# Optimization experiments

Measured on AMD Instinct MI355X. Metric: run time of the kernel, lower is better.

The kernel has to match this reference:

```python
import jax, jax.numpy as jnp
import numpy as np

EMBED_DIM = 768
NUM_HEADS = 12
HEAD_DIM = EMBED_DIM // NUM_HEADS
BSZ = 2
SEQ = 2048


def setup_inputs() -> dict:
    key = jax.random.key(0)
    ks = jax.random.split(key, 8)
    w = lambda k: (jax.random.normal(k, (EMBED_DIM, EMBED_DIM), jnp.float32) * 0.02)
    return {
        "hidden_states": jax.random.normal(ks[0], (BSZ, SEQ, EMBED_DIM), jnp.float32),
        "attention_mask": jnp.zeros((BSZ, 1, SEQ, SEQ), jnp.float32),
        "attention_bias": jax.random.normal(ks[1], (BSZ * NUM_HEADS, SEQ), jnp.float32),
        "Wq": w(ks[2]), "bq": jnp.zeros((EMBED_DIM,), jnp.float32),
        "Wk": w(ks[3]), "bk": jnp.zeros((EMBED_DIM,), jnp.float32),
        "Wv": w(ks[4]), "bv": jnp.zeros((EMBED_DIM,), jnp.float32),
        "Wo": w(ks[5]), "bo": jnp.zeros((EMBED_DIM,), jnp.float32),
        "beta": jnp.ones((1,), jnp.float32),
        "beta_bias": jnp.zeros((1,), jnp.float32),
    }


def reference(hidden_states, attention_mask, attention_bias, Wq, bq, Wk, bk, Wv, bv, Wo, bo, beta, beta_bias):
    b, t, e = hidden_states.shape
    scaling = HEAD_DIM ** -0.5
    split = lambda x: x.reshape(b, t, NUM_HEADS, HEAD_DIM).transpose(0, 2, 1, 3)  # b h t d
    q = split(hidden_states @ Wq.T + bq) * scaling
    k = split(hidden_states @ Wk.T + bk)
    v = split(hidden_states @ Wv.T + bv)
    # scores: [b, h, t, s]
    scores = jnp.einsum('bhqd,bhkd->bhqk', q, k)
    bias = attention_bias.reshape(b, NUM_HEADS, 1, t)  # (bsz*nh, src) -> broadcast over queries
    scores = scores + beta * bias + beta_bias + attention_mask
    probs = jax.nn.softmax(scores, axis=-1)
    out = jnp.einsum('bhqk,bhkd->bhqd', probs, v)  # b h t d
    out = out.transpose(0, 2, 1, 3).reshape(b, t, e)
    return out @ Wo.T + bo
```

## Files before the change

kernel.cpp:

```cpp
#include <hip/hip_runtime.h>
#include <hip/hip_bf16.h>

#define E 768
#define HD 64
#define NH 12
#define BSZ 2
#define SEQ 2048
#define M_ROWS (BSZ * SEQ)
#define BH (BSZ * NH)

#define LOG2E 1.44269504f
#define QSCALE 0.18033688f
#define MSHIFT 16.0f

typedef float f4_t __attribute__((ext_vector_type(4)));
typedef float f32x16 __attribute__((ext_vector_type(16)));
typedef __bf16 bf8_t __attribute__((ext_vector_type(8)));
typedef unsigned short us8_t __attribute__((ext_vector_type(8)));
typedef unsigned short us4_t __attribute__((ext_vector_type(4)));

__device__ inline unsigned short f2bf(float f) {
  union { float f; unsigned u; } v; v.f = f;
  unsigned u = v.u + 0x7FFFu + ((v.u >> 16) & 1u);
  return (unsigned short)(u >> 16);
}

__device__ inline float ex2(float x) { return __builtin_amdgcn_exp2f(x); }

__device__ inline float bflo(unsigned u) { union { unsigned u; float f; } v; v.u = u << 16; return v.f; }
__device__ inline float bfhi(unsigned u) { union { unsigned u; float f; } v; v.u = u & 0xFFFF0000u; return v.f; }

__device__ inline unsigned pk2(float a, float b) {
  union { float f; unsigned u; } ua, ub;
  ua.f = a; ub.f = b;
  return __builtin_amdgcn_perm(ub.u + 0x8000u, ua.u + 0x8000u, 0x07060302u);
}

__device__ inline void swap32(unsigned& a, unsigned& b) {
  asm volatile("v_permlane32_swap_b32 %0, %1" : "+v"(a), "+v"(b));
}

__global__ __launch_bounds__(256) void cvt_all(
    const float* __restrict__ X, const float* __restrict__ Wq,
    const float* __restrict__ Wk, const float* __restrict__ Wv,
    const float* __restrict__ Wo, const float* __restrict__ mask,
    const float* __restrict__ abias, const float* __restrict__ betaP,
    const float* __restrict__ bbiasP,
    unsigned short* __restrict__ Xbf, unsigned short* __restrict__ Wqkv,
    unsigned short* __restrict__ Wobf, unsigned short* __restrict__ maskbf,
    float* __restrict__ biasPf) {
  const int nW = E * E;
  int id = blockIdx.x;
  if (id < 2688) {
    const float* src;
    unsigned short* dst;
    float scale = 1.0f;
    int base;
    if (id < 1536) {
      src = X; dst = Xbf; base = id * 2048;
    } else {
      int r = id - 1536;
      int k = r / 288;
      int rb = r - k * 288;
      base = rb * 2048;
      if (k == 0)      { src = Wq; dst = Wqkv;          scale = QSCALE; }
      else if (k == 1) { src = Wk; dst = Wqkv + nW;     }
      else if (k == 2) { src = Wv; dst = Wqkv + 2 * nW; }
      else             { src = Wo; dst = Wobf;          }
    }
    int i = base + threadIdx.x * 8;
    const float4* s = (const float4*)(src + i);
    float4 a = s[0], b = s[1];
    us8_t o;
    o[0] = f2bf(a.x * scale); o[1] = f2bf(a.y * scale);
    o[2] = f2bf(a.z * scale); o[3] = f2bf(a.w * scale);
    o[4] = f2bf(b.x * scale); o[5] = f2bf(b.y * scale);
    o[6] = f2bf(b.z * scale); o[7] = f2bf(b.w * scale);
    *(us8_t*)(dst + i) = o;
    return;
  }
  if (id < 6784) {
    int rowid = id - 2688;
    int bb = rowid >> 11, q = rowid & 2047;
    int s0 = threadIdx.x * 8;
    const float4* s = (const float4*)(mask + (size_t)rowid * 2048 + s0);
    float4 a = s[0], c = s[1];
    int tile = s0 >> 6, kk = s0 & 63;
    int base = ((bb * 32 + tile) * 2048 + q) * 64 + (kk >> 5) * 32 + ((kk & 31) >> 3) * 4;
    us4_t lo, hi4;
    lo[0] = f2bf(a.x * LOG2E); lo[1] = f2bf(a.y * LOG2E);
    lo[2] = f2bf(a.z * LOG2E); lo[3] = f2bf(a.w * LOG2E);
    hi4[0] = f2bf(c.x * LOG2E); hi4[1] = f2bf(c.y * LOG2E);
    hi4[2] = f2bf(c.z * LOG2E); hi4[3] = f2bf(c.w * LOG2E);
    *(us4_t*)(maskbf + base) = lo;
    *(us4_t*)(maskbf + base + 16) = hi4;
    return;
  }
  {
    int bh = id - 6784;
    int s0 = threadIdx.x * 8;
    const float4* s = (const float4*)(abias + (size_t)bh * 2048 + s0);
    float4 a = s[0], c = s[1];
    float bv = LOG2E * betaP[0];
    float bc = LOG2E * bbiasP[0] - MSHIFT;
    int tile = s0 >> 6, kk = s0 & 63;
    int base = bh * 2048 + tile * 64 + (kk >> 5) * 32 + ((kk & 31) >> 3) * 4;
    f4_t lo = {fmaf(bv, a.x, bc), fmaf(bv, a.y, bc), fmaf(bv, a.z, bc), fmaf(bv, a.w, bc)};
    f4_t hi4 = {fmaf(bv, c.x, bc), fmaf(bv, c.y, bc), fmaf(bv, c.z, bc), fmaf(bv, c.w, bc)};
    *(f4_t*)(biasPf + base) = lo;
    *(f4_t*)(biasPf + base + 16) = hi4;
  }
}

__global__ __launch_bounds__(256) void gemm_qkv(
    const unsigned short* __restrict__ A, const unsigned short* __restrict__ Bw,
    const float* __restrict__ bq, const float* __restrict__ bk, const float* __restrict__ bv,
    unsigned short* __restrict__ Qb, unsigned short* __restrict__ Kb,
    unsigned short* __restrict__ Vtb) {
  __shared__ unsigned short Alds[64 * 64];
  __shared__ unsigned short Blds[128 * 64];
  const int w = threadIdx.x >> 6, lane = threadIdx.x & 63;
  const int quad = lane >> 4, l15 = lane & 15;
  const int rowBase = blockIdx.x * 64;
  const int colBase = blockIdx.y * 128;
  const int wr = (w & 1) * 32, wc = (w >> 1) * 64;
  f4_t acc[2][4] = {};
  const int swz = l15 & 7;

  for (int k0 = 0; k0 < E; k0 += 64) {
    __syncthreads();
#pragma unroll
    for (int c = 0; c < 2; ++c) {
      int s = c * 256 + w * 64 + lane;
      int r = s >> 3, col = ((s & 7) ^ (r & 7)) * 8;
      const unsigned short* ga = A + (size_t)(rowBase + r) * E + k0 + col;
      __builtin_amdgcn_global_load_lds((const __attribute__((address_space(1))) void*)ga,
          (__attribute__((address_space(3))) void*)&Alds[c * 2048 + w * 512], 16, 0, 0);
    }
#pragma unroll
    for (int c = 0; c < 4; ++c) {
      int s = c * 256 + w * 64 + lane;
      int r = s >> 3, col = ((s & 7) ^ (r & 7)) * 8;
      const unsigned short* gb = Bw + (size_t)(colBase + r) * E + k0 + col;
      __builtin_amdgcn_global_load_lds((const __attribute__((address_space(1))) void*)gb,
          (__attribute__((address_space(3))) void*)&Blds[c * 2048 + w * 512], 16, 0, 0);
    }
    __builtin_amdgcn_s_waitcnt(0);
    __syncthreads();
    bf8_t af[2][2], bfr[4][2];
#pragma unroll
    for (int mi = 0; mi < 2; ++mi)
#pragma unroll
      for (int ks = 0; ks < 2; ++ks)
        af[mi][ks] = *(const bf8_t*)&Alds[(wr + mi * 16 + l15) * 64 + (((ks * 4 + quad) ^ swz) << 3)];
#pragma unroll
    for (int ni = 0; ni < 4; ++ni)
#pragma unroll
      for (int ks = 0; ks < 2; ++ks)
        bfr[ni][ks] = *(const bf8_t*)&Blds[(wc + ni * 16 + l15) * 64 + (((ks * 4 + quad) ^ swz) << 3)];
#pragma unroll
    for (int ks = 0; ks < 2; ++ks)
#pragma unroll
      for (int mi = 0; mi < 2; ++mi)
#pragma unroll
        for (int ni = 0; ni < 4; ++ni)
          acc[mi][ni] = __builtin_amdgcn_mfma_f32_16x16x32_bf16(af[mi][ks], bfr[ni][ks], acc[mi][ni], 0, 0, 0);
  }

  const int which = colBase / E;
  __syncthreads();
  if (which < 2) {
    const float* biasP = (which == 0) ? bq : bk;
    unsigned short* dst = (which == 0) ? Qb : Kb;
    const float bscale = (which == 0) ? QSCALE : 1.0f;
    const int cnBase = colBase - which * E + wc;
    const int h = cnBase >> 6;
    float biasv[4];
#pragma unroll
    for (int ni = 0; ni < 4; ++ni) biasv[ni] = biasP[cnBase + ni * 16 + l15] * bscale;
    unsigned short* T = Blds + w * 1024;
    const int row = lane >> 2, colE = (lane & 3) * 16;
#pragma unroll
    for (int mi = 0; mi < 2; ++mi) {
#pragma unroll
      for (int ni = 0; ni < 4; ++ni)
#pragma unroll
        for (int r = 0; r < 4; ++r)
          T[(quad * 4 + r) * 64 + ni * 16 + l15] = f2bf(acc[mi][ni][r] + biasv[ni]);
      us8_t o0 = *(const us8_t*)&T[row * 64 + colE];
      us8_t o1 = *(const us8_t*)&T[row * 64 + colE + 8];
      int gm = rowBase + wr + mi * 16 + row;
      int b = gm >> 11, t = gm & 2047;
      unsigned short* drow = dst + ((size_t)(b * NH + h) * SEQ + t) * HD;
      *(us8_t*)&drow[colE] = o0;
      *(us8_t*)&drow[colE + 8] = o1;
    }
  } else {
#pragma unroll
    for (int mi = 0; mi < 2; ++mi) {
#pragma unroll
      for (int ni = 0; ni < 4; ++ni) {
        int cn = colBase - 2 * E + wc + ni * 16 + l15;
        int h = cn >> 6, d = cn & 63;
        float bias = bv[cn];
        int gm0 = rowBase + wr + mi * 16 + quad * 4;
        int b = gm0 >> 11, t = gm0 & 2047;
        us4_t o4;
#pragma unroll
        for (int r = 0; r < 4; ++r) o4[r] = f2bf(acc[mi][ni][r] + bias);
        *(us4_t*)&Vtb[((size_t)(b * NH + h) * HD + d) * SEQ + t] = o4;
      }
    }
  }
}

__device__ inline void addBM(f32x16& SA, const float* bp, us8_t ma, us8_t mb) {
  union { us8_t s; unsigned u[4]; } ca, cb;
  ca.s = ma; cb.s = mb;
#pragma unroll
  for (int g = 0; g < 4; ++g) {
    f4_t bw = *(const f4_t*)(bp + g * 4);
    unsigned wl = (g < 2) ? ca.u[2 * g] : cb.u[2 * g - 4];
    unsigned wh = (g < 2) ? ca.u[2 * g + 1] : cb.u[2 * g - 3];
    SA[4 * g + 0] += bw[0] + bflo(wl);
    SA[4 * g + 1] += bw[1] + bfhi(wl);
    SA[4 * g + 2] += bw[2] + bflo(wh);
    SA[4 * g + 3] += bw[3] + bfhi(wh);
  }
}

__device__ inline void packP(f32x16& SA, float& L, bf8_t& F0, bf8_t& F1) {
#pragma unroll
  for (int r = 0; r < 16; ++r) {
    SA[r] = ex2(SA[r]);
    L += SA[r];
  }
  unsigned u0 = pk2(SA[0], SA[1]), u1 = pk2(SA[2], SA[3]);
  unsigned u2 = pk2(SA[4], SA[5]), u3 = pk2(SA[6], SA[7]);
  unsigned u4 = pk2(SA[8], SA[9]), u5 = pk2(SA[10], SA[11]);
  unsigned u6 = pk2(SA[12], SA[13]), u7 = pk2(SA[14], SA[15]);
  swap32(u0, u2); swap32(u1, u3); swap32(u4, u6); swap32(u5, u7);
  union { unsigned u[4]; bf8_t b; } fa, fb;
  fa.u[0] = u0; fa.u[1] = u1; fa.u[2] = u2; fa.u[3] = u3;
  fb.u[0] = u4; fb.u[1] = u5; fb.u[2] = u6; fb.u[3] = u7;
  F0 = fa.b; F1 = fb.b;
}

__global__ __launch_bounds__(256, 3) void flash_attn12(
    const unsigned short* __restrict__ Qb, const unsigned short* __restrict__ Kb,
    const unsigned short* __restrict__ Vt, const unsigned short* __restrict__ maskP,
    const float* __restrict__ biasPf, unsigned short* __restrict__ attn) {
  __shared__ __align__(16) char smem[40960];
  const int tid = threadIdx.x;
  const int w = tid >> 6, lane = tid & 63;
  const int l31 = lane & 31, hi = lane >> 5;
  const int p = w >> 1, qw = (w & 1) * 32;
  const int id = blockIdx.x;
  const int h = id >> 6;
  const int qb = id & 63;
  const int qt = qb >> 1, b = qb & 1;
  const int bh = b * NH + h;
  const int q0 = qt * 64;
  const int q = q0 + qw + l31;

  unsigned short* KldsP = (unsigned short*)(smem + p * 16384);
  unsigned short* VldsP = KldsP + 4096;
  float* biasF = (float*)(smem + 32768);

  {
    const float* srcB = biasPf + bh * 2048 + tid * 8;
    f4_t b0 = *(const f4_t*)srcB;
    f4_t b1 = *(const f4_t*)(srcB + 4);
    *(f4_t*)&biasF[tid * 8] = b0;
    *(f4_t*)&biasF[tid * 8 + 4] = b1;
  }

  bf8_t qf[4];
  {
    const unsigned short* qbase = Qb + ((size_t)bh * SEQ + q) * HD + hi * 8;
#pragma unroll
    for (int dk = 0; dk < 4; ++dk) qf[dk] = *(const bf8_t*)(qbase + dk * 16);
  }

  const int li = (w & 1) * 64 + lane;
  const int r0 = li >> 3, cc = li & 7;
  const int dstOff = r0 * 64 + ((cc ^ (r0 & 7)) << 3);
  const unsigned short* KgBase = Kb + (size_t)bh * SEQ * HD;
  const unsigned short* VtG = Vt + (size_t)bh * HD * SEQ;
  const unsigned short* kSrc = KgBase + (p * 1024 + r0) * 64 + cc * 8;
  const unsigned short* vSrc = VtG + r0 * SEQ + p * 1024 + cc * 8;
  const unsigned short* mSrc = maskP + (((size_t)(b * 32 + p * 16) * 2048) + q) * 64 + hi * 16;

  us8_t kpf0, kpf1, kpf2, kpf3, vpf0, vpf1, vpf2, vpf3, mpf0, mpf1, mpf2, mpf3;

#define PF_KV(T)                                                              \
  {                                                                           \
    const unsigned short* kp_ = kSrc + (T) * 4096;                            \
    const unsigned short* vp_ = vSrc + (T) * 64;                              \
    asm volatile("global_load_dwordx4 %0, %4, off\n\t"                        \
                 "global_load_dwordx4 %1, %5, off\n\t"                        \
                 "global_load_dwordx4 %2, %6, off\n\t"                        \
                 "global_load_dwordx4 %3, %7, off"                            \
                 : "=&v"(kpf0), "=&v"(kpf1), "=&v"(kpf2), "=&v"(kpf3)         \
                 : "v"(kp_), "v"(kp_ + 1024), "v"(kp_ + 2048), "v"(kp_ + 3072)); \
    asm volatile("global_load_dwordx4 %0, %4, off\n\t"                        \
                 "global_load_dwordx4 %1, %5, off\n\t"                        \
                 "global_load_dwordx4 %2, %6, off\n\t"                        \
                 "global_load_dwordx4 %3, %7, off"                            \
                 : "=&v"(vpf0), "=&v"(vpf1), "=&v"(vpf2), "=&v"(vpf3)         \
                 : "v"(vp_), "v"(vp_ + 16 * SEQ), "v"(vp_ + 32 * SEQ),        \
                   "v"(vp_ + 48 * SEQ));                                      \
  }

#define PF_M(T)                                                               \
  {                                                                           \
    const unsigned short* mp_ = mSrc + (size_t)(T) * 131072;                  \
    asm volatile("global_load_dwordx4 %0, %4, off\n\t"                        \
                 "global_load_dwordx4 %1, %5, off\n\t"                        \
                 "global_load_dwordx4 %2, %6, off\n\t"                        \
                 "global_load_dwordx4 %3, %7, off"                            \
                 : "=&v"(mpf0), "=&v"(mpf1), "=&v"(mpf2), "=&v"(mpf3)         \
                 : "v"(mp_), "v"(mp_ + 8), "v"(mp_ + 32), "v"(mp_ + 40));     \
  }

  PF_KV(0);
  PF_M(0);

  f32x16 Oacc0 = {}, Oacc1 = {};
  float Lacc = 0.0f;
  const int swzA = l31 & 7;

  for (int it = 0; it < 16; ++it) {
    asm volatile("s_waitcnt vmcnt(4)"
                 : "+v"(kpf0), "+v"(kpf1), "+v"(kpf2), "+v"(kpf3),
                   "+v"(vpf0), "+v"(vpf1), "+v"(vpf2), "+v"(vpf3));
    __syncthreads();
    {
      us8_t* kd = (us8_t*)(KldsP + dstOff);
      kd[0] = kpf0; kd[128] = kpf1; kd[256] = kpf2; kd[384] = kpf3;
      us8_t* vd = (us8_t*)(VldsP + dstOff);
      vd[0] = vpf0; vd[128] = vpf1; vd[256] = vpf2; vd[384] = vpf3;
    }
    __syncthreads();

    f32x16 s0 = {}, s1 = {};
    __builtin_amdgcn_s_setprio(1);
#pragma unroll
    for (int dk = 0; dk < 4; ++dk) {
      const int co = ((dk * 2 + hi) ^ swzA) << 3;
      bf8_t k0 = *(const bf8_t*)(KldsP + l31 * 64 + co);
      bf8_t k1 = *(const bf8_t*)(KldsP + (32 + l31) * 64 + co);
      s0 = __builtin_amdgcn_mfma_f32_32x32x16_bf16(k0, qf[dk], s0, 0, 0, 0);
      s1 = __builtin_amdgcn_mfma_f32_32x32x16_bf16(k1, qf[dk], s1, 0, 0, 0);
    }
    __builtin_amdgcn_s_setprio(0);

    if (it < 15) {
      PF_KV(it + 1);
      asm volatile("s_waitcnt vmcnt(8)"
                   : "+v"(mpf0), "+v"(mpf1), "+v"(mpf2), "+v"(mpf3));
    } else {
      asm volatile("s_waitcnt vmcnt(0)"
                   : "+v"(mpf0), "+v"(mpf1), "+v"(mpf2), "+v"(mpf3));
    }

    const float* bp = biasF + ((p << 4) + it) * 64 + (hi << 4);
    addBM(s0, bp, mpf0, mpf1);
    addBM(s1, bp + 32, mpf2, mpf3);

    if (it < 15) PF_M(it + 1);

    bf8_t pfr0, pfr1, pfr2, pfr3;
    packP(s0, Lacc, pfr0, pfr1);
    packP(s1, Lacc, pfr2, pfr3);

    __builtin_amdgcn_s_setprio(1);
#pragma unroll
    for (int ks = 0; ks < 4; ++ks) {
      const int co = ((ks * 2 + hi) ^ swzA) << 3;
      bf8_t v0 = *(const bf8_t*)(VldsP + l31 * 64 + co);
      bf8_t v1 = *(const bf8_t*)(VldsP + (32 + l31) * 64 + co);
      bf8_t pp = ks == 0 ? pfr0 : ks == 1 ? pfr1 : ks == 2 ? pfr2 : pfr3;
      Oacc0 = __builtin_amdgcn_mfma_f32_32x32x16_bf16(v0, pp, Oacc0, 0, 0, 0);
      Oacc1 = __builtin_amdgcn_mfma_f32_32x32x16_bf16(v1, pp, Oacc1, 0, 0, 0);
    }
    __builtin_amdgcn_s_setprio(0);
  }

  __syncthreads();
  {
    float* OfP = (float*)smem + p * (64 * 65);
    const int qr = (qw + l31) * 65;
#pragma unroll
    for (int r = 0; r < 16; ++r) {
      int d = (r & 3) + 8 * (r >> 2) + 4 * hi;
      OfP[qr + d] = Oacc0[r];
      OfP[qr + 32 + d] = Oacc1[r];
    }
    float Lf = Lacc + __shfl_xor(Lacc, 32);
    if (hi == 0) OfP[qr + 64] = Lf;
  }
  __syncthreads();
  {
    const float* O0 = (const float*)smem;
    const float* O1 = O0 + 64 * 65;
    const int ql = tid >> 2, dc = tid & 3;
    const int qr = ql * 65;
    float inv = 1.0f / (O0[qr + 64] + O1[qr + 64]);
    unsigned short* orow = attn + ((size_t)b * SEQ + q0 + ql) * E + h * HD + dc * 16;
    us8_t o0, o1;
#pragma unroll
    for (int i = 0; i < 8; ++i)
      o0[i] = f2bf((O0[qr + dc * 16 + i] + O1[qr + dc * 16 + i]) * inv);
#pragma unroll
    for (int i = 0; i < 8; ++i)
      o1[i] = f2bf((O0[qr + dc * 16 + 8 + i] + O1[qr + dc * 16 + 8 + i]) * inv);
    *(us8_t*)orow = o0;
    *(us8_t*)(orow + 8) = o1;
  }
}

__global__ __launch_bounds__(256) void gemm_out(
    const unsigned short* __restrict__ A, const unsigned short* __restrict__ Bw,
    const float* __restrict__ bo, float* __restrict__ out) {
  __shared__ unsigned short Alds[64 * 64];
  __shared__ unsigned short Blds[64 * 64];
  const int w = threadIdx.x >> 6, lane = threadIdx.x & 63;
  const int quad = lane >> 4, l15 = lane & 15;
  const int rowBase = blockIdx.x * 64;
  const int colBase = blockIdx.y * 64;
  const int wr = (w & 1) * 32, wc = (w >> 1) * 32;
  f4_t acc[2][2] = {};
  const int swz = l15 & 7;

  for (int k0 = 0; k0 < E; k0 += 64) {
    __syncthreads();
#pragma unroll
    for (int c = 0; c < 2; ++c) {
      int s = c * 256 + w * 64 + lane;
      int r = s >> 3, col = ((s & 7) ^ (r & 7)) * 8;
      const unsigned short* ga = A + (size_t)(rowBase + r) * E + k0 + col;
      __builtin_amdgcn_global_load_lds((const __attribute__((address_space(1))) void*)ga,
          (__attribute__((address_space(3))) void*)&Alds[c * 2048 + w * 512], 16, 0, 0);
      const unsigned short* gb = Bw + (size_t)(colBase + r) * E + k0 + col;
      __builtin_amdgcn_global_load_lds((const __attribute__((address_space(1))) void*)gb,
          (__attribute__((address_space(3))) void*)&Blds[c * 2048 + w * 512], 16, 0, 0);
    }
    __builtin_amdgcn_s_waitcnt(0);
    __syncthreads();
    bf8_t af[2][2], bfr[2][2];
#pragma unroll
    for (int mi = 0; mi < 2; ++mi)
#pragma unroll
      for (int ks = 0; ks < 2; ++ks)
        af[mi][ks] = *(const bf8_t*)&Alds[(wr + mi * 16 + l15) * 64 + (((ks * 4 + quad) ^ swz) << 3)];
#pragma unroll
    for (int ni = 0; ni < 2; ++ni)
#pragma unroll
      for (int ks = 0; ks < 2; ++ks)
        bfr[ni][ks] = *(const bf8_t*)&Blds[(wc + ni * 16 + l15) * 64 + (((ks * 4 + quad) ^ swz) << 3)];
#pragma unroll
    for (int ks = 0; ks < 2; ++ks)
#pragma unroll
      for (int mi = 0; mi < 2; ++mi)
#pragma unroll
        for (int ni = 0; ni < 2; ++ni)
          acc[mi][ni] = __builtin_amdgcn_mfma_f32_16x16x32_bf16(af[mi][ks], bfr[ni][ks], acc[mi][ni], 0, 0, 0);
  }

#pragma unroll
  for (int mi = 0; mi < 2; ++mi) {
#pragma unroll
    for (int ni = 0; ni < 2; ++ni) {
      int gn = colBase + wc + ni * 16 + l15;
      float bias = bo[gn];
#pragma unroll
      for (int r = 0; r < 4; ++r) {
        int gm = rowBase + wr + mi * 16 + quad * 4 + r;
        out[(size_t)gm * E + gn] = acc[mi][ni][r] + bias;
      }
    }
  }
}

extern "C" void kernel_launch(void* const* d_in, const int* in_sizes, int n_in,
                              void* d_out, int out_size, void* d_ws, size_t ws_size,
                              hipStream_t stream) {
  const float* hidden = (const float*)d_in[0];
  const float* mask = (const float*)d_in[1];
  const float* abias = (const float*)d_in[2];
  const float* Wq = (const float*)d_in[3];
  const float* bq = (const float*)d_in[4];
  const float* Wk = (const float*)d_in[5];
  const float* bk = (const float*)d_in[6];
  const float* Wv = (const float*)d_in[7];
  const float* bv = (const float*)d_in[8];
  const float* Wo = (const float*)d_in[9];
  const float* bo = (const float*)d_in[10];
  const float* beta = (const float*)d_in[11];
  const float* betaBias = (const float*)d_in[12];
  float* out = (float*)d_out;

  char* ws = (char*)d_ws;
  unsigned short* Xbf = (unsigned short*)(ws);
  unsigned short* Wqkv = (unsigned short*)(ws + 6291456);
  unsigned short* Wobf = (unsigned short*)(ws + 9830400);
  unsigned short* Qbuf = (unsigned short*)(ws + 11010048);
  unsigned short* Kbuf = (unsigned short*)(ws + 17301504);
  unsigned short* Vtb = (unsigned short*)(ws + 23592960);
  unsigned short* Maskbf = (unsigned short*)(ws + 29884416);
  float* BiasP = (float*)(ws + 46661632);
  unsigned short* Attn = Xbf;

  cvt_all<<<6808, 256, 0, stream>>>(hidden, Wq, Wk, Wv, Wo, mask, abias, beta, betaBias,
                                    Xbf, Wqkv, Wobf, Maskbf, BiasP);
  gemm_qkv<<<dim3(64, 18), 256, 0, stream>>>(Xbf, Wqkv, bq, bk, bv, Qbuf, Kbuf, Vtb);
  flash_attn12<<<768, 256, 0, stream>>>(Qbuf, Kbuf, Vtb, Maskbf, BiasP, Attn);
  gemm_out<<<dim3(64, 12), 256, 0, stream>>>(Attn, Wobf, bo, out);
}
```

Before: 194.6 us.

## Read fp32 mask directly in attention; double-buffer LDS in both GEMMs

Removes the separate mask conversion pass, which wrote a bf16 tiled copy of the full mask, so the attention kernel now streams the fp32 mask straight from global memory and folds LOG2E scaling into the score initialisation, issuing mask loads before the QK MFMAs. This drops one full write and re-read of a large intermediate, at the cost of reading fp32 (twice the bytes) inside attention. The QKV and output GEMMs gain LDS double buffering so the next K-tile's global-to-LDS loads overlap the current MFMAs. The K/V prefetch is also reorganised with offset addressing and its wait points are moved.

New measurement: 245.4 us. +26.2%, slower.

```diff
diff --git a/kernel.cpp b/kernel.cpp
--- a/kernel.cpp
+++ b/kernel.cpp
@@ -27,9 +27,6 @@
 
 __device__ inline float ex2(float x) { return __builtin_amdgcn_exp2f(x); }
 
-__device__ inline float bflo(unsigned u) { union { unsigned u; float f; } v; v.u = u << 16; return v.f; }
-__device__ inline float bfhi(unsigned u) { union { unsigned u; float f; } v; v.u = u & 0xFFFF0000u; return v.f; }
-
 __device__ inline unsigned pk2(float a, float b) {
   union { float f; unsigned u; } ua, ub;
   ua.f = a; ub.f = b;
@@ -43,12 +40,10 @@
 __global__ __launch_bounds__(256) void cvt_all(
     const float* __restrict__ X, const float* __restrict__ Wq,
     const float* __restrict__ Wk, const float* __restrict__ Wv,
-    const float* __restrict__ Wo, const float* __restrict__ mask,
-    const float* __restrict__ abias, const float* __restrict__ betaP,
-    const float* __restrict__ bbiasP,
+    const float* __restrict__ Wo, const float* __restrict__ abias,
+    const float* __restrict__ betaP, const float* __restrict__ bbiasP,
     unsigned short* __restrict__ Xbf, unsigned short* __restrict__ Wqkv,
-    unsigned short* __restrict__ Wobf, unsigned short* __restrict__ maskbf,
-    float* __restrict__ biasPf) {
+    unsigned short* __restrict__ Wobf, float* __restrict__ biasPf) {
   const int nW = E * E;
   int id = blockIdx.x;
   if (id < 2688) {
@@ -79,25 +74,8 @@
     *(us8_t*)(dst + i) = o;
     return;
   }
-  if (id < 6784) {
-    int rowid = id - 2688;
-    int bb = rowid >> 11, q = rowid & 2047;
-    int s0 = threadIdx.x * 8;
-    const float4* s = (const float4*)(mask + (size_t)rowid * 2048 + s0);
-    float4 a = s[0], c = s[1];
-    int tile = s0 >> 6, kk = s0 & 63;
-    int base = ((bb * 32 + tile) * 2048 + q) * 64 + (kk >> 5) * 32 + ((kk & 31) >> 3) * 4;
-    us4_t lo, hi4;
-    lo[0] = f2bf(a.x * LOG2E); lo[1] = f2bf(a.y * LOG2E);
-    lo[2] = f2bf(a.z * LOG2E); lo[3] = f2bf(a.w * LOG2E);
-    hi4[0] = f2bf(c.x * LOG2E); hi4[1] = f2bf(c.y * LOG2E);
-    hi4[2] = f2bf(c.z * LOG2E); hi4[3] = f2bf(c.w * LOG2E);
-    *(us4_t*)(maskbf + base) = lo;
-    *(us4_t*)(maskbf + base + 16) = hi4;
-    return;
-  }
   {
-    int bh = id - 6784;
+    int bh = id - 2688;
     int s0 = threadIdx.x * 8;
     const float4* s = (const float4*)(abias + (size_t)bh * 2048 + s0);
     float4 a = s[0], c = s[1];
@@ -117,8 +95,8 @@
     const float* __restrict__ bq, const float* __restrict__ bk, const float* __restrict__ bv,
     unsigned short* __restrict__ Qb, unsigned short* __restrict__ Kb,
     unsigned short* __restrict__ Vtb) {
-  __shared__ unsigned short Alds[64 * 64];
-  __shared__ unsigned short Blds[128 * 64];
+  __shared__ unsigned short Alds[2][64 * 64];
+  __shared__ unsigned short Blds[2][128 * 64];
   const int w = threadIdx.x >> 6, lane = threadIdx.x & 63;
   const int quad = lane >> 4, l15 = lane & 15;
   const int rowBase = blockIdx.x * 64;
@@ -127,48 +105,57 @@
   f4_t acc[2][4] = {};
   const int swz = l15 & 7;
 
-  for (int k0 = 0; k0 < E; k0 += 64) {
-    __syncthreads();
-#pragma unroll
-    for (int c = 0; c < 2; ++c) {
-      int s = c * 256 + w * 64 + lane;
-      int r = s >> 3, col = ((s & 7) ^ (r & 7)) * 8;
-      const unsigned short* ga = A + (size_t)(rowBase + r) * E + k0 + col;
-      __builtin_amdgcn_global_load_lds((const __attribute__((address_space(1))) void*)ga,
-          (__attribute__((address_space(3))) void*)&Alds[c * 2048 + w * 512], 16, 0, 0);
-    }
-#pragma unroll
-    for (int c = 0; c < 4; ++c) {
-      int s = c * 256 + w * 64 + lane;
-      int r = s >> 3, col = ((s & 7) ^ (r & 7)) * 8;
-      const unsigned short* gb = Bw + (size_t)(colBase + r) * E + k0 + col;
-      __builtin_amdgcn_global_load_lds((const __attribute__((address_space(1))) void*)gb,
-          (__attribute__((address_space(3))) void*)&Blds[c * 2048 + w * 512], 16, 0, 0);
-    }
+#define STAGE_QKV(BUF, K0)                                                       \
+  {                                                                              \
+    const int kk0_ = (K0);                                                       \
+    for (int c = 0; c < 2; ++c) {                                                \
+      int s = c * 256 + w * 64 + lane;                                           \
+      int r = s >> 3, col = ((s & 7) ^ (r & 7)) * 8;                             \
+      const unsigned short* ga = A + (size_t)(rowBase + r) * E + kk0_ + col;     \
+      __builtin_amdgcn_global_load_lds(                                          \
+          (const __attribute__((address_space(1))) void*)ga,                     \
+          (__attribute__((address_space(3))) void*)&Alds[BUF][c * 2048 + w * 512], 16, 0, 0); \
+    }                                                                            \
+    for (int c = 0; c < 4; ++c) {                                                \
+      int s = c * 256 + w * 64 + lane;                                           \
+      int r = s >> 3, col = ((s & 7) ^ (r & 7)) * 8;                             \
+      const unsigned short* gb = Bw + (size_t)(colBase + r) * E + kk0_ + col;    \
+      __builtin_amdgcn_global_load_lds(                                          \
+          (const __attribute__((address_space(1))) void*)gb,                     \
+          (__attribute__((address_space(3))) void*)&Blds[BUF][c * 2048 + w * 512], 16, 0, 0); \
+    }                                                                            \
+  }
+
+  STAGE_QKV(0, 0);
+  __builtin_amdgcn_s_waitcnt(0);
+  __syncthreads();
+  for (int t = 0; t < 12; ++t) {
+    const int cur = t & 1;
+    if (t < 11) STAGE_QKV(cur ^ 1, (t + 1) * 64);
+    bf8_t af[2][2], bfr[4][2];
+#pragma unroll
+    for (int mi = 0; mi < 2; ++mi)
+#pragma unroll
+      for (int ks = 0; ks < 2; ++ks)
+        af[mi][ks] = *(const bf8_t*)&Alds[cur][(wr + mi * 16 + l15) * 64 + (((ks * 4 + quad) ^ swz) << 3)];
+#pragma unroll
+    for (int ni = 0; ni < 4; ++ni)
+#pragma unroll
+      for (int ks = 0; ks < 2; ++ks)
+        bfr[ni][ks] = *(const bf8_t*)&Blds[cur][(wc + ni * 16 + l15) * 64 + (((ks * 4 + quad) ^ swz) << 3)];
+#pragma unroll
+    for (int ks = 0; ks < 2; ++ks)
+#pragma unroll
+      for (int mi = 0; mi < 2; ++mi)
+#pragma unroll
+        for (int ni = 0; ni < 4; ++ni)
+          acc[mi][ni] = __builtin_amdgcn_mfma_f32_16x16x32_bf16(af[mi][ks], bfr[ni][ks], acc[mi][ni], 0, 0, 0);
     __builtin_amdgcn_s_waitcnt(0);
     __syncthreads();
-    bf8_t af[2][2], bfr[4][2];
-#pragma unroll
-    for (int mi = 0; mi < 2; ++mi)
-#pragma unroll
-      for (int ks = 0; ks < 2; ++ks)
-        af[mi][ks] = *(const bf8_t*)&Alds[(wr + mi * 16 + l15) * 64 + (((ks * 4 + quad) ^ swz) << 3)];
-#pragma unroll
-    for (int ni = 0; ni < 4; ++ni)
-#pragma unroll
-      for (int ks = 0; ks < 2; ++ks)
-        bfr[ni][ks] = *(const bf8_t*)&Blds[(wc + ni * 16 + l15) * 64 + (((ks * 4 + quad) ^ swz) << 3)];
-#pragma unroll
-    for (int ks = 0; ks < 2; ++ks)
-#pragma unroll
-      for (int mi = 0; mi < 2; ++mi)
-#pragma unroll
-        for (int ni = 0; ni < 4; ++ni)
-          acc[mi][ni] = __builtin_amdgcn_mfma_f32_16x16x32_bf16(af[mi][ks], bfr[ni][ks], acc[mi][ni], 0, 0, 0);
-  }
+  }
+#undef STAGE_QKV
 
   const int which = colBase / E;
-  __syncthreads();
   if (which < 2) {
     const float* biasP = (which == 0) ? bq : bk;
     unsigned short* dst = (which == 0) ? Qb : Kb;
@@ -178,7 +165,7 @@
     float biasv[4];
 #pragma unroll
     for (int ni = 0; ni < 4; ++ni) biasv[ni] = biasP[cnBase + ni * 16 + l15] * bscale;
-    unsigned short* T = Blds + w * 1024;
+    unsigned short* T = &Blds[0][0] + w * 1024;
     const int row = lane >> 2, colE = (lane & 3) * 16;
 #pragma unroll
     for (int mi = 0; mi < 2; ++mi) {
@@ -214,18 +201,14 @@
   }
 }
 
-__device__ inline void addBM(f32x16& SA, const float* bp, us8_t ma, us8_t mb) {
-  union { us8_t s; unsigned u[4]; } ca, cb;
-  ca.s = ma; cb.s = mb;
+__device__ inline void initS(f32x16& SA, const float* bp, f4_t m0, f4_t m1,
+                             f4_t m2, f4_t m3) {
 #pragma unroll
   for (int g = 0; g < 4; ++g) {
+    f4_t mg = (g == 0) ? m0 : (g == 1) ? m1 : (g == 2) ? m2 : m3;
     f4_t bw = *(const f4_t*)(bp + g * 4);
-    unsigned wl = (g < 2) ? ca.u[2 * g] : cb.u[2 * g - 4];
-    unsigned wh = (g < 2) ? ca.u[2 * g + 1] : cb.u[2 * g - 3];
-    SA[4 * g + 0] += bw[0] + bflo(wl);
-    SA[4 * g + 1] += bw[1] + bfhi(wl);
-    SA[4 * g + 2] += bw[2] + bflo(wh);
-    SA[4 * g + 3] += bw[3] + bfhi(wh);
+#pragma unroll
+    for (int j = 0; j < 4; ++j) SA[4 * g + j] = fmaf(LOG2E, mg[j], bw[j]);
   }
 }
 
@@ -246,9 +229,9 @@
   F0 = fa.b; F1 = fb.b;
 }
 
-__global__ __launch_bounds__(256, 3) void flash_attn12(
+__global__ __launch_bounds__(256, 3) void flash_attn14(
     const unsigned short* __restrict__ Qb, const unsigned short* __restrict__ Kb,
-    const unsigned short* __restrict__ Vt, const unsigned short* __restrict__ maskP,
+    const unsigned short* __restrict__ Vt, const float* __restrict__ maskF,
     const float* __restrict__ biasPf, unsigned short* __restrict__ attn) {
   __shared__ __align__(16) char smem[40960];
   const int tid = threadIdx.x;
@@ -269,10 +252,8 @@
 
   {
     const float* srcB = biasPf + bh * 2048 + tid * 8;
-    f4_t b0 = *(const f4_t*)srcB;
-    f4_t b1 = *(const f4_t*)(srcB + 4);
-    *(f4_t*)&biasF[tid * 8] = b0;
-    *(f4_t*)&biasF[tid * 8 + 4] = b1;
+    *(f4_t*)&biasF[tid * 8] = *(const f4_t*)srcB;
+    *(f4_t*)&biasF[tid * 8 + 4] = *(const f4_t*)(srcB + 4);
   }
 
   bf8_t qf[4];
@@ -285,53 +266,50 @@
   const int li = (w & 1) * 64 + lane;
   const int r0 = li >> 3, cc = li & 7;
   const int dstOff = r0 * 64 + ((cc ^ (r0 & 7)) << 3);
-  const unsigned short* KgBase = Kb + (size_t)bh * SEQ * HD;
+  const unsigned short* kb0 = Kb + (size_t)bh * SEQ * HD + (p * 1024 + r0) * 64 + cc * 8;
   const unsigned short* VtG = Vt + (size_t)bh * HD * SEQ;
-  const unsigned short* kSrc = KgBase + (p * 1024 + r0) * 64 + cc * 8;
-  const unsigned short* vSrc = VtG + r0 * SEQ + p * 1024 + cc * 8;
-  const unsigned short* mSrc = maskP + (((size_t)(b * 32 + p * 16) * 2048) + q) * 64 + hi * 16;
-
-  us8_t kpf0, kpf1, kpf2, kpf3, vpf0, vpf1, vpf2, vpf3, mpf0, mpf1, mpf2, mpf3;
-
-#define PF_KV(T)                                                              \
-  {                                                                           \
-    const unsigned short* kp_ = kSrc + (T) * 4096;                            \
-    const unsigned short* vp_ = vSrc + (T) * 64;                              \
-    asm volatile("global_load_dwordx4 %0, %4, off\n\t"                        \
-                 "global_load_dwordx4 %1, %5, off\n\t"                        \
-                 "global_load_dwordx4 %2, %6, off\n\t"                        \
-                 "global_load_dwordx4 %3, %7, off"                            \
-                 : "=&v"(kpf0), "=&v"(kpf1), "=&v"(kpf2), "=&v"(kpf3)         \
-                 : "v"(kp_), "v"(kp_ + 1024), "v"(kp_ + 2048), "v"(kp_ + 3072)); \
-    asm volatile("global_load_dwordx4 %0, %4, off\n\t"                        \
-                 "global_load_dwordx4 %1, %5, off\n\t"                        \
-                 "global_load_dwordx4 %2, %6, off\n\t"                        \
-                 "global_load_dwordx4 %3, %7, off"                            \
-                 : "=&v"(vpf0), "=&v"(vpf1), "=&v"(vpf2), "=&v"(vpf3)         \
-                 : "v"(vp_), "v"(vp_ + 16 * SEQ), "v"(vp_ + 32 * SEQ),        \
-                   "v"(vp_ + 48 * SEQ));                                      \
-  }
-
-#define PF_M(T)                                                               \
-  {                                                                           \
-    const unsigned short* mp_ = mSrc + (size_t)(T) * 131072;                  \
-    asm volatile("global_load_dwordx4 %0, %4, off\n\t"                        \
-                 "global_load_dwordx4 %1, %5, off\n\t"                        \
-                 "global_load_dwordx4 %2, %6, off\n\t"                        \
-                 "global_load_dwordx4 %3, %7, off"                            \
-                 : "=&v"(mpf0), "=&v"(mpf1), "=&v"(mpf2), "=&v"(mpf3)         \
-                 : "v"(mp_), "v"(mp_ + 8), "v"(mp_ + 32), "v"(mp_ + 40));     \
-  }
-
-  PF_KV(0);
-  PF_M(0);
+  const unsigned short* vb0 = VtG + (size_t)r0 * SEQ + p * 1024 + cc * 8;
+  const float* mp = maskF + ((size_t)b * SEQ + q) * SEQ + p * 1024 + hi * 4;
+
+  us8_t kpf0, kpf1, kpf2, kpf3, vpf0, vpf1, vpf2, vpf3;
+  f4_t mq0, mq1, mq2, mq3, mq4, mq5, mq6, mq7;
+
+#define PF_KV()                                                               \
+  asm volatile("global_load_dwordx4 %0, %8, off\n\t"                          \
+               "global_load_dwordx4 %1, %8, off offset:2048\n\t"              \
+               "global_load_dwordx4 %2, %9, off\n\t"                          \
+               "global_load_dwordx4 %3, %9, off offset:2048\n\t"              \
+               "global_load_dwordx4 %4, %10, off\n\t"                         \
+               "global_load_dwordx4 %5, %11, off\n\t"                         \
+               "global_load_dwordx4 %6, %12, off\n\t"                         \
+               "global_load_dwordx4 %7, %13, off"                             \
+               : "=&v"(kpf0), "=&v"(kpf1), "=&v"(kpf2), "=&v"(kpf3),          \
+                 "=&v"(vpf0), "=&v"(vpf1), "=&v"(vpf2), "=&v"(vpf3)           \
+               : "v"(kb0), "v"(kb0 + 2048), "v"(vb0), "v"(vb0 + 16 * SEQ),    \
+                 "v"(vb0 + 32 * SEQ), "v"(vb0 + 48 * SEQ))
+
+#define PF_M()                                                                \
+  asm volatile("global_load_dwordx4 %0, %8, off\n\t"                          \
+               "global_load_dwordx4 %1, %8, off offset:32\n\t"                \
+               "global_load_dwordx4 %2, %8, off offset:64\n\t"                \
+               "global_load_dwordx4 %3, %8, off offset:96\n\t"                \
+               "global_load_dwordx4 %4, %8, off offset:128\n\t"               \
+               "global_load_dwordx4 %5, %8, off offset:160\n\t"               \
+               "global_load_dwordx4 %6, %8, off offset:192\n\t"               \
+               "global_load_dwordx4 %7, %8, off offset:224"                   \
+               : "=&v"(mq0), "=&v"(mq1), "=&v"(mq2), "=&v"(mq3),              \
+                 "=&v"(mq4), "=&v"(mq5), "=&v"(mq6), "=&v"(mq7)               \
+               : "v"(mp))
+
+  PF_KV();
+  PF_M();
 
   f32x16 Oacc0 = {}, Oacc1 = {};
   float Lacc = 0.0f;
   const int swzA = l31 & 7;
 
   for (int it = 0; it < 16; ++it) {
-    asm volatile("s_waitcnt vmcnt(4)"
+    asm volatile("s_waitcnt vmcnt(8)"
                  : "+v"(kpf0), "+v"(kpf1), "+v"(kpf2), "+v"(kpf3),
                    "+v"(vpf0), "+v"(vpf1), "+v"(vpf2), "+v"(vpf3));
     __syncthreads();
@@ -343,7 +321,25 @@
     }
     __syncthreads();
 
-    f32x16 s0 = {}, s1 = {};
+    if (it < 15) {
+      kb0 += 4096; vb0 += 64;
+      PF_KV();
+      asm volatile("s_waitcnt vmcnt(8)"
+                   : "+v"(mq0), "+v"(mq1), "+v"(mq2), "+v"(mq3),
+                     "+v"(mq4), "+v"(mq5), "+v"(mq6), "+v"(mq7));
+    } else {
+      asm volatile("s_waitcnt vmcnt(0)"
+                   : "+v"(mq0), "+v"(mq1), "+v"(mq2), "+v"(mq3),
+                     "+v"(mq4), "+v"(mq5), "+v"(mq6), "+v"(mq7));
+    }
+
+    const float* bp = biasF + ((p << 4) + it) * 64 + (hi << 4);
+    f32x16 s0, s1;
+    initS(s0, bp, mq0, mq1, mq2, mq3);
+    initS(s1, bp + 32, mq4, mq5, mq6, mq7);
+
+    if (it < 15) { mp += 64; PF_M(); }
+
     __builtin_amdgcn_s_setprio(1);
 #pragma unroll
     for (int dk = 0; dk < 4; ++dk) {
@@ -354,21 +350,6 @@
       s1 = __builtin_amdgcn_mfma_f32_32x32x16_bf16(k1, qf[dk], s1, 0, 0, 0);
     }
     __builtin_amdgcn_s_setprio(0);
-
-    if (it < 15) {
-      PF_KV(it + 1);
-      asm volatile("s_waitcnt vmcnt(8)"
-                   : "+v"(mpf0), "+v"(mpf1), "+v"(mpf2), "+v"(mpf3));
-    } else {
-      asm volatile("s_waitcnt vmcnt(0)"
-                   : "+v"(mpf0), "+v"(mpf1), "+v"(mpf2), "+v"(mpf3));
-    }
-
-    const float* bp = biasF + ((p << 4) + it) * 64 + (hi << 4);
-    addBM(s0, bp, mpf0, mpf1);
-    addBM(s1, bp + 32, mpf2, mpf3);
-
-    if (it < 15) PF_M(it + 1);
 
     bf8_t pfr0, pfr1, pfr2, pfr3;
     packP(s0, Lacc, pfr0, pfr1);
@@ -386,6 +367,8 @@
     }
     __builtin_amdgcn_s_setprio(0);
   }
+#undef PF_KV
+#undef PF_M
 
   __syncthreads();
   {
@@ -423,8 +406,8 @@
 __global__ __launch_bounds__(256) void gemm_out(
     const unsigned short* __restrict__ A, const unsigned short* __restrict__ Bw,
     const float* __restrict__ bo, float* __restrict__ out) {
-  __shared__ unsigned short Alds[64 * 64];
-  __shared__ unsigned short Blds[64 * 64];
+  __shared__ unsigned short Alds[2][64 * 64];
+  __shared__ unsigned short Blds[2][64 * 64];
   const int w = threadIdx.x >> 6, lane = threadIdx.x & 63;
   const int quad = lane >> 4, l15 = lane & 15;
   const int rowBase = blockIdx.x * 64;
@@ -433,40 +416,51 @@
   f4_t acc[2][2] = {};
   const int swz = l15 & 7;
 
-  for (int k0 = 0; k0 < E; k0 += 64) {
-    __syncthreads();
-#pragma unroll
-    for (int c = 0; c < 2; ++c) {
-      int s = c * 256 + w * 64 + lane;
-      int r = s >> 3, col = ((s & 7) ^ (r & 7)) * 8;
-      const unsigned short* ga = A + (size_t)(rowBase + r) * E + k0 + col;
-      __builtin_amdgcn_global_load_lds((const __attribute__((address_space(1))) void*)ga,
-          (__attribute__((address_space(3))) void*)&Alds[c * 2048 + w * 512], 16, 0, 0);
-      const unsigned short* gb = Bw + (size_t)(colBase + r) * E + k0 + col;
-      __builtin_amdgcn_global_load_lds((const __attribute__((address_space(1))) void*)gb,
-          (__attribute__((address_space(3))) void*)&Blds[c * 2048 + w * 512], 16, 0, 0);
-    }
+#define STAGE_OUT(BUF, K0)                                                       \
+  {                                                                              \
+    const int kk0_ = (K0);                                                       \
+    for (int c = 0; c < 2; ++c) {                                                \
+      int s = c * 256 + w * 64 + lane;                                           \
+      int r = s >> 3, col = ((s & 7) ^ (r & 7)) * 8;                             \
+      const unsigned short* ga = A + (size_t)(rowBase + r) * E + kk0_ + col;     \
+      __builtin_amdgcn_global_load_lds(                                          \
+          (const __attribute__((address_space(1))) void*)ga,                     \
+          (__attribute__((address_space(3))) void*)&Alds[BUF][c * 2048 + w * 512], 16, 0, 0); \
+      const unsigned short* gb = Bw + (size_t)(colBase + r) * E + kk0_ + col;    \
+      __builtin_amdgcn_global_load_lds(                                          \
+          (const __attribute__((address_space(1))) void*)gb,                     \
+          (__attribute__((address_space(3))) void*)&Blds[BUF][c * 2048 + w * 512], 16, 0, 0); \
+    }                                                                            \
+  }
+
+  STAGE_OUT(0, 0);
+  __builtin_amdgcn_s_waitcnt(0);
+  __syncthreads();
+  for (int t = 0; t < 12; ++t) {
+    const int cur = t & 1;
+    if (t < 11) STAGE_OUT(cur ^ 1, (t + 1) * 64);
+    bf8_t af[2][2], bfr[2][2];
+#pragma unroll
+    for (int mi = 0; mi < 2; ++mi)
+#pragma unroll
+      for (int ks = 0; ks < 2; ++ks)
+        af[mi][ks] = *(const bf8_t*)&Alds[cur][(wr + mi * 16 + l15) * 64 + (((ks * 4 + quad) ^ swz) << 3)];
+#pragma unroll
+    for (int ni = 0; ni < 2; ++ni)
+#pragma unroll
+      for (int ks = 0; ks < 2; ++ks)
+        bfr[ni][ks] = *(const bf8_t*)&Blds[cur][(wc + ni * 16 + l15) * 64 + (((ks * 4 + quad) ^ swz) << 3)];
+#pragma unroll
+    for (int ks = 0; ks < 2; ++ks)
+#pragma unroll
+      for (int mi = 0; mi < 2; ++mi)
+#pragma unroll
+        for (int ni = 0; ni < 2; ++ni)
+          acc[mi][ni] = __builtin_amdgcn_mfma_f32_16x16x32_bf16(af[mi][ks], bfr[ni][ks], acc[mi][ni], 0, 0, 0);
     __builtin_amdgcn_s_waitcnt(0);
     __syncthreads();
-    bf8_t af[2][2], bfr[2][2];
-#pragma unroll
-    for (int mi = 0; mi < 2; ++mi)
-#pragma unroll
-      for (int ks = 0; ks < 2; ++ks)
-        af[mi][ks] = *(const bf8_t*)&Alds[(wr + mi * 16 + l15) * 64 + (((ks * 4 + quad) ^ swz) << 3)];
-#pragma unroll
-    for (int ni = 0; ni < 2; ++ni)
-#pragma unroll
-      for (int ks = 0; ks < 2; ++ks)
-        bfr[ni][ks] = *(const bf8_t*)&Blds[(wc + ni * 16 + l15) * 64 + (((ks * 4 + quad) ^ swz) << 3)];
-#pragma unroll
-    for (int ks = 0; ks < 2; ++ks)
-#pragma unroll
-      for (int mi = 0; mi < 2; ++mi)
-#pragma unroll
-        for (int ni = 0; ni < 2; ++ni)
-          acc[mi][ni] = __builtin_amdgcn_mfma_f32_16x16x32_bf16(af[mi][ks], bfr[ni][ks], acc[mi][ni], 0, 0, 0);
-  }
+  }
+#undef STAGE_OUT
 
 #pragma unroll
   for (int mi = 0; mi < 2; ++mi) {
@@ -508,13 +502,12 @@
   unsigned short* Qbuf = (unsigned short*)(ws + 11010048);
   unsigned short* Kbuf = (unsigned short*)(ws + 17301504);
   unsigned short* Vtb = (unsigned short*)(ws + 23592960);
-  unsigned short* Maskbf = (unsigned short*)(ws + 29884416);
   float* BiasP = (float*)(ws + 46661632);
   unsigned short* Attn = Xbf;
 
-  cvt_all<<<6808, 256, 0, stream>>>(hidden, Wq, Wk, Wv, Wo, mask, abias, beta, betaBias,
-                                    Xbf, Wqkv, Wobf, Maskbf, BiasP);
+  cvt_all<<<2712, 256, 0, stream>>>(hidden, Wq, Wk, Wv, Wo, abias, beta, betaBias,
+                                    Xbf, Wqkv, Wobf, BiasP);
   gemm_qkv<<<dim3(64, 18), 256, 0, stream>>>(Xbf, Wqkv, bq, bk, bv, Qbuf, Kbuf, Vtb);
-  flash_attn12<<<768, 256, 0, stream>>>(Qbuf, Kbuf, Vtb, Maskbf, BiasP, Attn);
+  flash_attn14<<<768, 256, 0, stream>>>(Qbuf, Kbuf, Vtb, mask, BiasP, Attn);
   gemm_out<<<dim3(64, 12), 256, 0, stream>>>(Attn, Wobf, bo, out);
 }
```
